# Optimization experiments

Measured on AMD Instinct MI355X. Metric: run time of the kernel, lower is better.

The kernel has to match this reference:

```python
import jax, jax.numpy as jnp
import numpy as np

B, T, E, A = 4, 4096, 1024, 1024

def setup_inputs() -> dict:
    key = jax.random.key(0)
    k1, k2, k3, k4 = jax.random.split(key, 4)
    scale = 1.0 / np.sqrt(E)  # ~ nn.Linear default init scale
    return {
        "embedded": jax.random.normal(k1, (B, T, E), dtype=jnp.float32),
        "Wq": jax.random.uniform(k2, (A, E), jnp.float32, -scale, scale),
        "Wk": jax.random.uniform(k3, (A, E), jnp.float32, -scale, scale),
        "Wv": jax.random.uniform(k4, (A, E), jnp.float32, -scale, scale),
    }

def reference(embedded, Wq, Wk, Wv):
    # QKV projections (nn.Linear without bias: x @ W.T)
    q = jnp.einsum('bte,ae->bta', embedded, Wq)
    k = jnp.einsum('bte,ae->bta', embedded, Wk)
    v = jnp.einsum('bte,ae->bta', embedded, Wv)
    A_dim = q.shape[-1]
    # scaled scores [B, T, T]
    scores = jnp.einsum('bqa,bka->bqk', q, k) / jnp.sqrt(jnp.float32(A_dim))
    # causal mask (lower triangular allowed)
    Tq = scores.shape[-1]
    causal = jnp.tril(jnp.ones((Tq, Tq), dtype=bool))
    scores = jnp.where(causal, scores, -jnp.inf)
    probs = jax.nn.softmax(scores, axis=-1)
    out = jnp.einsum('bqk,bka->bqa', probs, v)
    return jnp.round(out, 4)
```

## Files before the change

kernel.cpp:

```cpp
#include <hip/hip_runtime.h>
#include <hip/hip_bf16.h>

using bf16 = __hip_bfloat16;

typedef __attribute__((ext_vector_type(4))) float f32x4;
typedef __attribute__((ext_vector_type(8))) short short8;

typedef const void __attribute__((address_space(1)))* gas1_t;
typedef void __attribute__((address_space(3)))* las3_t;
#define GLDS(gp, lp) __builtin_amdgcn_global_load_lds((gas1_t)(gp), (las3_t)(lp), 16, 0, 0)

__device__ inline short f2bfbits(float f) {
  union { bf16 h; short s; } u;
  u.h = __float2bfloat16(f);
  return u.s;
}
__device__ inline float bf2f(short u) {
  unsigned x = ((unsigned)(unsigned short)u) << 16;
  float f; __builtin_memcpy(&f, &x, 4); return f;
}

__device__ inline void store_out(float* C, size_t idx, float v) { C[idx] = v; }
__device__ inline void store_out(bf16* C, size_t idx, float v) { C[idx] = __float2bfloat16(v); }

template<typename TOUT, int MODE>
__global__ __launch_bounds__(256) void gemm_bt(
    const short* __restrict__ A, int lda, size_t sAz,
    const short* __restrict__ B, int ldb, size_t sBz,
    TOUT* __restrict__ C, int ldc, size_t sCz,
    int K, float scale)
{
  int bx, by, z;
  if constexpr (MODE == 1) {
    const int i = blockIdx.x;
    by = (int)((__builtin_sqrtf(8.f * (float)i + 1.f) - 1.f) * 0.5f);
    if (((by * (by + 1)) >> 1) > i) by--;
    else if ((((by + 1) * (by + 2)) >> 1) <= i) by++;
    bx = i - ((by * (by + 1)) >> 1);
    z = blockIdx.z;
  } else if constexpr (MODE == 2) {
    const int w = blockIdx.x;
    const int c = w & 255, k = w >> 8;
    bx = c & 7;
    const int g = c >> 3;
    by = (k & 1) ? 31 - g : g;
    z = ((k & 1) << 1) | (k >> 1);
  } else {
    bx = blockIdx.x; by = blockIdx.y; z = blockIdx.z;
  }
  const int tri_by = (by * (by + 1)) >> 1;

  A += (size_t)z * sAz;
  B += (size_t)z * sBz;
  C += (size_t)z * sCz;

  int Klen = K;
  if (MODE == 2) Klen = min(K, (by + 1) * 128);

  __shared__ short a_lds[128 * 32];
  __shared__ short b_lds[128 * 32];

  const int t = threadIdx.x;
  const int lane = t & 63;
  const int wave = t >> 6;
  const int wm = wave >> 1, wn = wave & 1;
  const int fr = lane & 15, kh = lane >> 4;

  f32x4 acc[4][4];
  #pragma unroll
  for (int i = 0; i < 4; i++)
    #pragma unroll
    for (int j = 0; j < 4; j++) acc[i][j] = (f32x4){0.f, 0.f, 0.f, 0.f};

  for (int k0 = 0; k0 < Klen; k0 += 32) {
    #pragma unroll
    for (int i = 0; i < 2; i++) {
      int e = i * 256 + t;
      int r_ = e >> 2, c_ = (e & 3) * 8;
      const short* pa;
      if constexpr (MODE == 2)
        pa = A + ((size_t)(tri_by + (k0 >> 7))) * 16384 + (size_t)r_ * 128 + (k0 & 127) + c_;
      else
        pa = A + (size_t)(by * 128 + r_) * lda + k0 + c_;
      const short* pb = B + (size_t)(bx * 128 + r_) * ldb + k0 + c_;
      GLDS(pa, (char*)a_lds + i * 4096 + wave * 1024);
      GLDS(pb, (char*)b_lds + i * 4096 + wave * 1024);
    }
    __syncthreads();

    short8 af[4], bfr[4];
    #pragma unroll
    for (int m = 0; m < 4; m++)
      af[m] = *(const short8*)&a_lds[(wm * 64 + m * 16 + fr) * 32 + kh * 8];
    #pragma unroll
    for (int n = 0; n < 4; n++)
      bfr[n] = *(const short8*)&b_lds[(wn * 64 + n * 16 + fr) * 32 + kh * 8];
    #pragma unroll
    for (int m = 0; m < 4; m++)
      #pragma unroll
      for (int n = 0; n < 4; n++)
        acc[m][n] = __builtin_amdgcn_mfma_f32_16x16x32_bf16(af[m], bfr[n], acc[m][n], 0, 0, 0);
    __syncthreads();
  }

  #pragma unroll
  for (int m = 0; m < 4; m++)
    #pragma unroll
    for (int n = 0; n < 4; n++) {
      int col_l = wn * 64 + n * 16 + fr;
      #pragma unroll
      for (int r = 0; r < 4; r++) {
        int row_l = wm * 64 + m * 16 + kh * 4 + r;
        if constexpr (MODE == 1)
          store_out(C, (size_t)(tri_by + bx) * 16384 + (size_t)row_l * 128 + col_l,
                    acc[m][n][r] * scale);
        else
          store_out(C, (size_t)(by * 128 + row_l) * ldc + bx * 128 + col_l,
                    acc[m][n][r] * scale);
      }
    }
}

__global__ __launch_bounds__(256) void cvt_bf16(
    const float* __restrict__ in, bf16* __restrict__ out, int n, float scale)
{
  for (int i = (blockIdx.x * 256 + threadIdx.x) * 8; i < n; i += gridDim.x * 2048) {
    f32x4 v0 = *(const f32x4*)&in[i];
    f32x4 v1 = *(const f32x4*)&in[i + 4];
    short8 o = { f2bfbits(v0[0] * scale), f2bfbits(v0[1] * scale),
                 f2bfbits(v0[2] * scale), f2bfbits(v0[3] * scale),
                 f2bfbits(v1[0] * scale), f2bfbits(v1[1] * scale),
                 f2bfbits(v1[2] * scale), f2bfbits(v1[3] * scale) };
    *(short8*)&out[i] = o;
  }
}

__global__ __launch_bounds__(256) void softmax_causal_packed(short* SP, int T)
{
  __shared__ float rowv[4096];
  __shared__ float red[4];
  const int r = blockIdx.x;
  const int z = blockIdx.y;
  const int rb = r >> 7, rl = r & 127;
  const size_t tri = (size_t)((rb * (rb + 1)) >> 1);
  short* base = SP + (size_t)z * 528 * 16384;
  const int L = r + 1;
  const int kend = (rb + 1) * 128;
  const int t = threadIdx.x;

  float lmax = -3.0e38f;
  for (int i = t * 8; i < kend; i += 2048) {
    short8 s = *(const short8*)(base + (tri + (i >> 7)) * 16384 + (size_t)rl * 128 + (i & 127));
    #pragma unroll
    for (int j = 0; j < 8; j++) {
      float v = bf2f(s[j]);
      rowv[i + j] = v;
      if (i + j < L) lmax = fmaxf(lmax, v);
    }
  }
  #pragma unroll
  for (int o = 32; o > 0; o >>= 1) lmax = fmaxf(lmax, __shfl_down(lmax, o));
  if ((t & 63) == 0) red[t >> 6] = lmax;
  __syncthreads();
  const float m = fmaxf(fmaxf(red[0], red[1]), fmaxf(red[2], red[3]));
  __syncthreads();

  float lsum = 0.f;
  for (int i = t; i < kend; i += 256) {
    float e = (i < L) ? __expf(rowv[i] - m) : 0.f;
    rowv[i] = e;
    lsum += e;
  }
  #pragma unroll
  for (int o = 32; o > 0; o >>= 1) lsum += __shfl_down(lsum, o);
  if ((t & 63) == 0) red[t >> 6] = lsum;
  __syncthreads();
  const float inv = 1.f / (red[0] + red[1] + red[2] + red[3]);

  for (int i = t * 8; i < kend; i += 2048) {
    short8 o;
    #pragma unroll
    for (int j = 0; j < 8; j++) o[j] = f2bfbits(rowv[i + j] * inv);
    *(short8*)(base + (tri + (i >> 7)) * 16384 + (size_t)rl * 128 + (i & 127)) = o;
  }
}

extern "C" void kernel_launch(void* const* d_in, const int* in_sizes, int n_in,
                              void* d_out, int out_size, void* d_ws, size_t ws_size,
                              hipStream_t stream) {
  (void)in_sizes; (void)n_in; (void)out_size; (void)ws_size;
  const float* X  = (const float*)d_in[0];
  const float* Wq = (const float*)d_in[1];
  const float* Wk = (const float*)d_in[2];
  const float* Wv = (const float*)d_in[3];
  float* Out = (float*)d_out;

  const int Bn = 4, T = 4096, E = 1024, Ad = 1024;
  const int M = Bn * T;

  char* ws = (char*)d_ws;
  short* QKb = (short*)ws;
  short* Vt  = (short*)(ws + 67108864);
  short* Xb  = (short*)(ws + 100663296);
  short* Wqk = (short*)(ws + 134217728);
  short* Wvb = (short*)(ws + 138412032);
  short* SP  = (short*)(ws + 100663296);

  dim3 blk(256);
  const float qscale = 0.03125f;
  const size_t SPz = (size_t)528 * 16384;

  cvt_bf16<<<dim3(8192), blk, 0, stream>>>(X, (bf16*)Xb, M * E, 1.0f);
  cvt_bf16<<<dim3(512),  blk, 0, stream>>>(Wq, (bf16*)Wqk, Ad * E, qscale);
  cvt_bf16<<<dim3(512),  blk, 0, stream>>>(Wk, (bf16*)(Wqk + (size_t)Ad * E), Ad * E, 1.0f);
  cvt_bf16<<<dim3(512),  blk, 0, stream>>>(Wv, (bf16*)Wvb, Ad * E, 1.0f);

  gemm_bt<bf16, 0><<<dim3(2048 / 128, M / 128), blk, 0, stream>>>(
      Xb, E, 0, Wqk, E, 0, (bf16*)QKb, 2048, 0, E, 1.0f);
  gemm_bt<bf16, 0><<<dim3(M / 128, Ad / 128), blk, 0, stream>>>(
      Wvb, E, 0, Xb, E, 0, (bf16*)Vt, M, 0, E, 1.0f);

  gemm_bt<bf16, 1><<<dim3(528, 1, Bn), blk, 0, stream>>>(
      QKb, 2048, (size_t)T * 2048,
      QKb + 1024, 2048, (size_t)T * 2048,
      (bf16*)SP, 128, SPz, Ad, 1.0f);

  softmax_causal_packed<<<dim3(T, Bn), blk, 0, stream>>>(SP, T);

  gemm_bt<float, 2><<<dim3(1024), blk, 0, stream>>>(
      SP, 128, SPz,
      Vt, M, (size_t)T,
      Out, Ad, (size_t)T * Ad, T, 1.0f);
}
```

Baseline: 450.6 us.

## Double-buffer GEMM LDS tiles, swizzle LDS layout, and remap block tile order

The GEMM main loop now keeps two LDS buffers, so global-to-LDS loads for the next K tile are issued while MFMAs run on the current one, with one barrier per iteration instead of two. Source columns are XOR-swizzled at load time to reduce LDS bank conflicts on fragment reads. Wave priority is raised around the MFMA block. Block-to-tile mapping is remapped for the QK projection (grouped rows) and for the V projection (new MODE 3, column-major walk) to improve L2 reuse. The cost is doubled LDS use per block, which may lower occupancy.

After: 424.2 us. 5.9% less time.

```diff
diff --git a/kernel.cpp b/kernel.cpp
--- a/kernel.cpp
+++ b/kernel.cpp
@@ -45,8 +45,17 @@
     const int g = c >> 3;
     by = (k & 1) ? 31 - g : g;
     z = ((k & 1) << 1) | (k >> 1);
+  } else if constexpr (MODE == 0) {
+    const int f = blockIdx.y * gridDim.x + blockIdx.x;
+    by = ((f >> 7) << 3) | ((f >> 4) & 7);
+    bx = f & 15;
+    z = blockIdx.z;
   } else {
-    bx = blockIdx.x; by = blockIdx.y; z = blockIdx.z;
+    const int f = blockIdx.y * gridDim.x + blockIdx.x;
+    const int gy = gridDim.y;
+    by = f % gy;
+    bx = f / gy;
+    z = blockIdx.z;
   }
   const int tri_by = (by * (by + 1)) >> 1;
 
@@ -56,15 +65,18 @@
 
   int Klen = K;
   if (MODE == 2) Klen = min(K, (by + 1) * 128);
-
-  __shared__ short a_lds[128 * 32];
-  __shared__ short b_lds[128 * 32];
+  const int NT = Klen >> 5;
+
+  __shared__ short a_lds[2][128 * 32];
+  __shared__ short b_lds[2][128 * 32];
 
   const int t = threadIdx.x;
   const int lane = t & 63;
   const int wave = t >> 6;
   const int wm = wave >> 1, wn = wave & 1;
   const int fr = lane & 15, kh = lane >> 4;
+  const int sx = (fr >> 1) & 3;
+  const int koff = ((kh ^ sx) << 3);
 
   f32x4 acc[4][4];
   #pragma unroll
@@ -72,35 +84,54 @@
     #pragma unroll
     for (int j = 0; j < 4; j++) acc[i][j] = (f32x4){0.f, 0.f, 0.f, 0.f};
 
-  for (int k0 = 0; k0 < Klen; k0 += 32) {
+  auto STAGE = [&](int kt) {
+    const int buf = kt & 1;
+    const int k0 = kt * 32;
     #pragma unroll
     for (int i = 0; i < 2; i++) {
       int e = i * 256 + t;
-      int r_ = e >> 2, c_ = (e & 3) * 8;
+      int row = e >> 2, c = e & 3;
+      int sc = ((c ^ ((row >> 1) & 3)) << 3);
       const short* pa;
       if constexpr (MODE == 2)
-        pa = A + ((size_t)(tri_by + (k0 >> 7))) * 16384 + (size_t)r_ * 128 + (k0 & 127) + c_;
+        pa = A + ((size_t)(tri_by + (k0 >> 7))) * 16384 + (size_t)row * 128 + (k0 & 127) + sc;
       else
-        pa = A + (size_t)(by * 128 + r_) * lda + k0 + c_;
-      const short* pb = B + (size_t)(bx * 128 + r_) * ldb + k0 + c_;
-      GLDS(pa, (char*)a_lds + i * 4096 + wave * 1024);
-      GLDS(pb, (char*)b_lds + i * 4096 + wave * 1024);
+        pa = A + (size_t)(by * 128 + row) * lda + k0 + sc;
+      const short* pb = B + (size_t)(bx * 128 + row) * ldb + k0 + sc;
+      GLDS(pa, (char*)&a_lds[buf][0] + i * 4096 + wave * 1024);
+      GLDS(pb, (char*)&b_lds[buf][0] + i * 4096 + wave * 1024);
     }
-    __syncthreads();
+  };
+
+  STAGE(0);
+  asm volatile("s_waitcnt vmcnt(0)\ns_barrier" ::: "memory");
+
+  for (int kt = 0; kt < NT; kt++) {
+    const short* as = &a_lds[kt & 1][0];
+    const short* bs = &b_lds[kt & 1][0];
+
+    if (kt + 1 < NT) STAGE(kt + 1);
 
     short8 af[4], bfr[4];
     #pragma unroll
     for (int m = 0; m < 4; m++)
-      af[m] = *(const short8*)&a_lds[(wm * 64 + m * 16 + fr) * 32 + kh * 8];
+      af[m] = *(const short8*)&as[(wm * 64 + m * 16 + fr) * 32 + koff];
     #pragma unroll
     for (int n = 0; n < 4; n++)
-      bfr[n] = *(const short8*)&b_lds[(wn * 64 + n * 16 + fr) * 32 + kh * 8];
+      bfr[n] = *(const short8*)&bs[(wn * 64 + n * 16 + fr) * 32 + koff];
+
+    asm volatile("s_waitcnt lgkmcnt(0)" ::: "memory");
+    __builtin_amdgcn_sched_barrier(0);
+    __builtin_amdgcn_s_setprio(1);
     #pragma unroll
     for (int m = 0; m < 4; m++)
       #pragma unroll
       for (int n = 0; n < 4; n++)
         acc[m][n] = __builtin_amdgcn_mfma_f32_16x16x32_bf16(af[m], bfr[n], acc[m][n], 0, 0, 0);
-    __syncthreads();
+    __builtin_amdgcn_s_setprio(0);
+
+    if (kt + 1 < NT)
+      asm volatile("s_waitcnt vmcnt(0)\ns_barrier" ::: "memory");
   }
 
   #pragma unroll
@@ -217,7 +248,7 @@
 
   gemm_bt<bf16, 0><<<dim3(2048 / 128, M / 128), blk, 0, stream>>>(
       Xb, E, 0, Wqk, E, 0, (bf16*)QKb, 2048, 0, E, 1.0f);
-  gemm_bt<bf16, 0><<<dim3(M / 128, Ad / 128), blk, 0, stream>>>(
+  gemm_bt<bf16, 3><<<dim3(M / 128, Ad / 128), blk, 0, stream>>>(
       Wvb, E, 0, Xb, E, 0, (bf16*)Vt, M, 0, E, 1.0f);
 
   gemm_bt<bf16, 1><<<dim3(528, 1, Bn), blk, 0, stream>>>(
```

## Move all GEMMs to 256x256 tiles with a triple-buffered swizzled LDS pipeline

Applied to the files above, without the earlier changes.

Replaces the 128x128, 256-thread GEMM with a 256x256, 512-thread kernel. Each wave now holds an 8x4 set of MFMA accumulators. Global-to-LDS loads are triple-buffered two k-steps ahead and overlapped with MFMA phases through split A/B staging, explicit waitcnt/barrier and s_setprio, and LDS columns are XOR-swizzled to avoid bank conflicts. The packed causal score layout, softmax and PV GEMM are adapted to 256-row blocks, and the PV GEMM drops its load-balancing schedule for a plain 3D grid. This raises data reuse and compute overlap, at the cost of more masked causal work per tile, fewer blocks and heavy LDS use per CU.

After: 399.2 us. 11.4% less time.

```diff
diff --git a/kernel.cpp b/kernel.cpp
--- a/kernel.cpp
+++ b/kernel.cpp
@@ -24,30 +24,23 @@
 __device__ inline void store_out(bf16* C, size_t idx, float v) { C[idx] = __float2bfloat16(v); }
 
 template<typename TOUT, int MODE>
-__global__ __launch_bounds__(256) void gemm_bt(
+__global__ __launch_bounds__(512, 2) void gemm256(
     const short* __restrict__ A, int lda, size_t sAz,
     const short* __restrict__ B, int ldb, size_t sBz,
     TOUT* __restrict__ C, int ldc, size_t sCz,
     int K, float scale)
 {
-  int bx, by, z;
+  int bx, by;
   if constexpr (MODE == 1) {
     const int i = blockIdx.x;
     by = (int)((__builtin_sqrtf(8.f * (float)i + 1.f) - 1.f) * 0.5f);
     if (((by * (by + 1)) >> 1) > i) by--;
     else if ((((by + 1) * (by + 2)) >> 1) <= i) by++;
     bx = i - ((by * (by + 1)) >> 1);
-    z = blockIdx.z;
-  } else if constexpr (MODE == 2) {
-    const int w = blockIdx.x;
-    const int c = w & 255, k = w >> 8;
-    bx = c & 7;
-    const int g = c >> 3;
-    by = (k & 1) ? 31 - g : g;
-    z = ((k & 1) << 1) | (k >> 1);
   } else {
-    bx = blockIdx.x; by = blockIdx.y; z = blockIdx.z;
-  }
+    bx = blockIdx.x; by = blockIdx.y;
+  }
+  const int z = blockIdx.z;
   const int tri_by = (by * (by + 1)) >> 1;
 
   A += (size_t)z * sAz;
@@ -55,67 +48,116 @@
   C += (size_t)z * sCz;
 
   int Klen = K;
-  if (MODE == 2) Klen = min(K, (by + 1) * 128);
-
-  __shared__ short a_lds[128 * 32];
-  __shared__ short b_lds[128 * 32];
+  if (MODE == 2) Klen = min(K, (by + 1) * 256);
+  const int NT = Klen >> 5;
+
+  __shared__ short As[3][256 * 32];
+  __shared__ short Bs[3][256 * 32];
 
   const int t = threadIdx.x;
   const int lane = t & 63;
   const int wave = t >> 6;
-  const int wm = wave >> 1, wn = wave & 1;
+  const int wm = wave >> 2;
+  const int wn = wave & 3;
   const int fr = lane & 15, kh = lane >> 4;
-
-  f32x4 acc[4][4];
-  #pragma unroll
-  for (int i = 0; i < 4; i++)
+  const int koff = ((kh ^ ((fr >> 1) & 3)) << 3);
+
+  int srow[2], scol[2];
+  #pragma unroll
+  for (int j = 0; j < 2; j++) {
+    int e = j * 512 + t;
+    srow[j] = e >> 2;
+    scol[j] = (((e & 3) ^ ((e >> 3) & 3)) << 3);
+  }
+
+  f32x4 acc[8][4];
+  #pragma unroll
+  for (int i = 0; i < 8; i++)
     #pragma unroll
     for (int j = 0; j < 4; j++) acc[i][j] = (f32x4){0.f, 0.f, 0.f, 0.f};
 
-  for (int k0 = 0; k0 < Klen; k0 += 32) {
-    #pragma unroll
-    for (int i = 0; i < 2; i++) {
-      int e = i * 256 + t;
-      int r_ = e >> 2, c_ = (e & 3) * 8;
+  auto STAGE_A = [&](int kt) {
+    const int buf = kt % 3, k0 = kt * 32;
+    #pragma unroll
+    for (int j = 0; j < 2; j++) {
       const short* pa;
       if constexpr (MODE == 2)
-        pa = A + ((size_t)(tri_by + (k0 >> 7))) * 16384 + (size_t)r_ * 128 + (k0 & 127) + c_;
+        pa = A + (size_t)(tri_by + (k0 >> 8)) * 65536 + (size_t)srow[j] * 256 + (k0 & 255) + scol[j];
       else
-        pa = A + (size_t)(by * 128 + r_) * lda + k0 + c_;
-      const short* pb = B + (size_t)(bx * 128 + r_) * ldb + k0 + c_;
-      GLDS(pa, (char*)a_lds + i * 4096 + wave * 1024);
-      GLDS(pb, (char*)b_lds + i * 4096 + wave * 1024);
-    }
-    __syncthreads();
-
+        pa = A + (size_t)(by * 256 + srow[j]) * lda + k0 + scol[j];
+      GLDS(pa, (char*)&As[buf][0] + j * 8192 + wave * 1024);
+    }
+  };
+  auto STAGE_B = [&](int kt) {
+    const int buf = kt % 3, k0 = kt * 32;
+    #pragma unroll
+    for (int j = 0; j < 2; j++) {
+      const short* pb = B + (size_t)(bx * 256 + srow[j]) * ldb + k0 + scol[j];
+      GLDS(pb, (char*)&Bs[buf][0] + j * 8192 + wave * 1024);
+    }
+  };
+
+  STAGE_A(0); STAGE_B(0);
+  STAGE_A(1); STAGE_B(1);
+  asm volatile("s_waitcnt vmcnt(4)\ns_barrier" ::: "memory");
+
+  const int arow = wm * 128 + fr;
+  const int brow = wn * 64 + fr;
+
+  for (int kt = 0; kt < NT; kt++) {
+    const short* as = &As[kt % 3][0];
+    const short* bs = &Bs[kt % 3][0];
     short8 af[4], bfr[4];
-    #pragma unroll
-    for (int m = 0; m < 4; m++)
-      af[m] = *(const short8*)&a_lds[(wm * 64 + m * 16 + fr) * 32 + kh * 8];
-    #pragma unroll
-    for (int n = 0; n < 4; n++)
-      bfr[n] = *(const short8*)&b_lds[(wn * 64 + n * 16 + fr) * 32 + kh * 8];
+
+    #pragma unroll
+    for (int n = 0; n < 4; n++) bfr[n] = *(const short8*)&bs[(brow + n * 16) * 32 + koff];
+    #pragma unroll
+    for (int m = 0; m < 4; m++) af[m] = *(const short8*)&as[(arow + m * 16) * 32 + koff];
+    if (kt + 2 < NT) STAGE_A(kt + 2);
+    __builtin_amdgcn_s_barrier();
+    asm volatile("s_waitcnt lgkmcnt(0)" ::: "memory");
+    __builtin_amdgcn_sched_barrier(0);
+    __builtin_amdgcn_s_setprio(1);
     #pragma unroll
     for (int m = 0; m < 4; m++)
       #pragma unroll
       for (int n = 0; n < 4; n++)
         acc[m][n] = __builtin_amdgcn_mfma_f32_16x16x32_bf16(af[m], bfr[n], acc[m][n], 0, 0, 0);
-    __syncthreads();
-  }
-
-  #pragma unroll
-  for (int m = 0; m < 4; m++)
+    __builtin_amdgcn_s_setprio(0);
+    __builtin_amdgcn_sched_barrier(0);
+
+    #pragma unroll
+    for (int m = 0; m < 4; m++) af[m] = *(const short8*)&as[(arow + (m + 4) * 16) * 32 + koff];
+    if (kt + 2 < NT) STAGE_B(kt + 2);
+    __builtin_amdgcn_s_barrier();
+    asm volatile("s_waitcnt lgkmcnt(0)" ::: "memory");
+    __builtin_amdgcn_sched_barrier(0);
+    __builtin_amdgcn_s_setprio(1);
+    #pragma unroll
+    for (int m = 0; m < 4; m++)
+      #pragma unroll
+      for (int n = 0; n < 4; n++)
+        acc[m + 4][n] = __builtin_amdgcn_mfma_f32_16x16x32_bf16(af[m], bfr[n], acc[m + 4][n], 0, 0, 0);
+    __builtin_amdgcn_s_setprio(0);
+    __builtin_amdgcn_sched_barrier(0);
+
+    if (kt + 2 < NT)      asm volatile("s_waitcnt vmcnt(4)\ns_barrier" ::: "memory");
+    else if (kt + 1 < NT) asm volatile("s_waitcnt vmcnt(0)\ns_barrier" ::: "memory");
+  }
+
+  #pragma unroll
+  for (int m = 0; m < 8; m++)
     #pragma unroll
     for (int n = 0; n < 4; n++) {
       int col_l = wn * 64 + n * 16 + fr;
       #pragma unroll
       for (int r = 0; r < 4; r++) {
-        int row_l = wm * 64 + m * 16 + kh * 4 + r;
+        int row_l = wm * 128 + m * 16 + kh * 4 + r;
         if constexpr (MODE == 1)
-          store_out(C, (size_t)(tri_by + bx) * 16384 + (size_t)row_l * 128 + col_l,
+          store_out(C, (size_t)(tri_by + bx) * 65536 + (size_t)row_l * 256 + col_l,
                     acc[m][n][r] * scale);
         else
-          store_out(C, (size_t)(by * 128 + row_l) * ldc + bx * 128 + col_l,
+          store_out(C, (size_t)(by * 256 + row_l) * ldc + bx * 256 + col_l,
                     acc[m][n][r] * scale);
       }
     }
@@ -141,16 +183,16 @@
   __shared__ float red[4];
   const int r = blockIdx.x;
   const int z = blockIdx.y;
-  const int rb = r >> 7, rl = r & 127;
+  const int rb = r >> 8, rl = r & 255;
   const size_t tri = (size_t)((rb * (rb + 1)) >> 1);
-  short* base = SP + (size_t)z * 528 * 16384;
+  short* base = SP + (size_t)z * 136 * 65536;
   const int L = r + 1;
-  const int kend = (rb + 1) * 128;
+  const int kend = (rb + 1) * 256;
   const int t = threadIdx.x;
 
   float lmax = -3.0e38f;
   for (int i = t * 8; i < kend; i += 2048) {
-    short8 s = *(const short8*)(base + (tri + (i >> 7)) * 16384 + (size_t)rl * 128 + (i & 127));
+    short8 s = *(const short8*)(base + (tri + (i >> 8)) * 65536 + (size_t)rl * 256 + (i & 255));
     #pragma unroll
     for (int j = 0; j < 8; j++) {
       float v = bf2f(s[j]);
@@ -181,7 +223,7 @@
     short8 o;
     #pragma unroll
     for (int j = 0; j < 8; j++) o[j] = f2bfbits(rowv[i + j] * inv);
-    *(short8*)(base + (tri + (i >> 7)) * 16384 + (size_t)rl * 128 + (i & 127)) = o;
+    *(short8*)(base + (tri + (i >> 8)) * 65536 + (size_t)rl * 256 + (i & 255)) = o;
   }
 }
 
@@ -206,29 +248,29 @@
   short* Wvb = (short*)(ws + 138412032);
   short* SP  = (short*)(ws + 100663296);
 
-  dim3 blk(256);
+  dim3 blk(256), blk5(512);
   const float qscale = 0.03125f;
-  const size_t SPz = (size_t)528 * 16384;
+  const size_t SPz = (size_t)136 * 65536;
 
   cvt_bf16<<<dim3(8192), blk, 0, stream>>>(X, (bf16*)Xb, M * E, 1.0f);
   cvt_bf16<<<dim3(512),  blk, 0, stream>>>(Wq, (bf16*)Wqk, Ad * E, qscale);
   cvt_bf16<<<dim3(512),  blk, 0, stream>>>(Wk, (bf16*)(Wqk + (size_t)Ad * E), Ad * E, 1.0f);
   cvt_bf16<<<dim3(512),  blk, 0, stream>>>(Wv, (bf16*)Wvb, Ad * E, 1.0f);
 
-  gemm_bt<bf16, 0><<<dim3(2048 / 128, M / 128), blk, 0, stream>>>(
+  gemm256<bf16, 0><<<dim3(2048 / 256, M / 256), blk5, 0, stream>>>(
       Xb, E, 0, Wqk, E, 0, (bf16*)QKb, 2048, 0, E, 1.0f);
-  gemm_bt<bf16, 0><<<dim3(M / 128, Ad / 128), blk, 0, stream>>>(
+  gemm256<bf16, 0><<<dim3(M / 256, Ad / 256), blk5, 0, stream>>>(
       Wvb, E, 0, Xb, E, 0, (bf16*)Vt, M, 0, E, 1.0f);
 
-  gemm_bt<bf16, 1><<<dim3(528, 1, Bn), blk, 0, stream>>>(
+  gemm256<bf16, 1><<<dim3(136, 1, Bn), blk5, 0, stream>>>(
       QKb, 2048, (size_t)T * 2048,
       QKb + 1024, 2048, (size_t)T * 2048,
-      (bf16*)SP, 128, SPz, Ad, 1.0f);
+      (bf16*)SP, 256, SPz, Ad, 1.0f);
 
   softmax_causal_packed<<<dim3(T, Bn), blk, 0, stream>>>(SP, T);
 
-  gemm_bt<float, 2><<<dim3(1024), blk, 0, stream>>>(
-      SP, 128, SPz,
+  gemm256<float, 2><<<dim3(Ad / 256, T / 256, Bn), blk5, 0, stream>>>(
+      SP, 256, SPz,
       Vt, M, (size_t)T,
       Out, Ad, (size_t)T * Ad, T, 1.0f);
 }
```
